# Performance work log

Hardware: AMD Instinct MI355X
Metric: run time of the kernel (lower is better)

The kernel has to match this reference:

```python
import jax, jax.numpy as jnp
import numpy as np
import math

NZ, NX, NY = 4, 2048, 2048
DX = DY = 4000.0


def dstI1D(x):
    # type-I discrete sine transform along last axis (ortho norm) via irfft
    n = x.shape[-1]
    pad = [(0, 0)] * (x.ndim - 1) + [(1, 1)]
    return jnp.fft.irfft(-1j * jnp.pad(x, pad), axis=-1, norm='ortho')[..., 1:n + 1]


def dstI2D(x):
    # DST-I over the last two axes
    x = dstI1D(x)
    x = jnp.swapaxes(dstI1D(jnp.swapaxes(x, -1, -2)), -1, -2)
    return x


def inverse_elliptic_dstI(f, helmholtz_dst):
    # DST-I is its own inverse with ortho norm: solve in spectral space
    return dstI2D(dstI2D(f) / helmholtz_dst)


def center_avg_2D(x):
    return 0.25 * (x[..., 1:, 1:] + x[..., 1:, :-1] + x[..., :-1, 1:] + x[..., :-1, :-1])


def _build_solver_constants(beta):
    # create_helmholtz_dst
    x, y = jnp.meshgrid(jnp.arange(1, NY), jnp.arange(1, NX), indexing='ij')
    L_mat = (2 * (jnp.cos(math.pi / NX * x) - 1) / DX ** 2
             + 2 * (jnp.cos(math.pi / NY * y) - 1) / DY ** 2)
    H_mat = (L_mat[None] - beta[:, None, None]).astype(jnp.float32)  # [Nz, Nx-1, Ny-1]
    # compute_homogeneous_solution
    ones_int = jnp.ones((NZ, NX - 1, NY - 1), jnp.float32)
    sol = inverse_elliptic_dstI(ones_int, H_mat)
    sol = jnp.pad(sol, ((0, 0), (1, 1), (1, 1)))  # [Nz, Nx+1, Ny+1]
    homsol = jnp.ones((NZ, NX + 1, NY + 1), jnp.float32) + sol * beta[:, None, None]
    homsol_mean = jnp.mean(center_avg_2D(homsol), axis=(-2, -1))  # mask = all ones
    return H_mat, homsol.astype(jnp.float32), homsol_mean.astype(jnp.float32)


def setup_inputs() -> dict:
    key = jax.random.key(0)
    k1, k2 = jax.random.split(key)
    q = jax.random.normal(k1, (NZ, NX - 1, NY - 1), jnp.float32)
    # mode<->layer change of basis (Mode2LayerTransformer): Cm2l = inv(Cl2m)
    A = jax.random.normal(k2, (NZ, NZ), jnp.float32) * 0.3 + jnp.eye(NZ, dtype=jnp.float32)
    Cl2m = A
    Cm2l = jnp.linalg.inv(A).astype(jnp.float32)
    # lambda_sq eigenvalues (1/deformation-radius^2), first barotropic mode ~ 0
    beta = jnp.array([0.0, 1.0e-9, 4.0e-9, 1.0e-8], jnp.float32)
    H_mat, homsol, homsol_mean = _build_solver_constants(beta)
    return {'q': q, 'Cl2m': Cl2m, 'Cm2l': Cm2l,
            'helmholtz_mat': H_mat, 'homsol': homsol, 'homsol_mean': homsol_mean}


def reference(q, Cl2m, Cm2l, helmholtz_mat, homsol, homsol_mean):
    # layer -> mode
    src_modes = jnp.einsum('ml,lxy->mxy', Cl2m, q)
    # spectral elliptic solve per mode (Nz batched over leading axis)
    psi_modes = inverse_elliptic_dstI(src_modes, helmholtz_mat)
    psi_modes = jnp.pad(psi_modes, ((0, 0), (1, 1), (1, 1)))  # [Nz, Nx+1, Ny+1]
    # homogeneous-solution correction to enforce zero mean
    psi_modes_mean = jnp.mean(center_avg_2D(psi_modes), axis=(-2, -1))
    alpha = -psi_modes_mean / homsol_mean
    psi_modes = psi_modes + alpha[:, None, None] * homsol
    # mode -> layer
    psi = jnp.einsum('lm,mxy->lxy', Cm2l, psi_modes)
    return psi
```

## Files before the change

kernel.cpp:

```cpp
#include <hip/hip_runtime.h>


typedef __attribute__((ext_vector_type(8))) short bf16x8;
typedef __attribute__((ext_vector_type(4))) float f32x4;
typedef __attribute__((ext_vector_type(8))) unsigned short ushort8;

#define LDS_SPACE __attribute__((address_space(3)))
#define GLB_SPACE __attribute__((address_space(1)))

__device__ __forceinline__ void gld_lds16(const unsigned short* g, unsigned short* l) {
  __builtin_amdgcn_global_load_lds((const GLB_SPACE void*)g, (LDS_SPACE void*)l, 16, 0, 0);
}

__device__ __forceinline__ bf16x8 ds_read128(const void* p) {
  bf16x8 r;
  const LDS_SPACE char* lp = (const LDS_SPACE char*)p;
  asm volatile("ds_read_b128 %0, %1" : "=v"(r) : "v"(lp));
  return r;
}

__device__ __forceinline__ float sinrev(float rev) {
  float r;
  asm("v_sin_f32 %0, %1" : "=v"(r) : "v"(rev));
  return r;
}

__device__ __forceinline__ unsigned short f2b(float f) {
  union { float f; unsigned u; } v; v.f = f;
  unsigned r = (v.u + 0x7fffu + ((v.u >> 16) & 1u)) >> 16;
  return (unsigned short)r;
}
__device__ __forceinline__ float b2f(unsigned short u) {
  union { unsigned u; float f; } v; v.u = ((unsigned)u) << 16;
  return v.f;
}

#define LGKM(N) asm volatile("s_waitcnt lgkmcnt(" #N ")" ::: "memory")
#define VMC(N)  asm volatile("s_waitcnt vmcnt(" #N ")" ::: "memory")
#define BAR()   __builtin_amdgcn_s_barrier()
#define SB0()   __builtin_amdgcn_sched_barrier(0)
#define PRIO1() __builtin_amdgcn_s_setprio(1)
#define PRIO0() __builtin_amdgcn_s_setprio(0)

__global__ __launch_bounds__(256)
void tables_kernel(unsigned short* __restrict__ T) {
  const int idx = blockIdx.x * 256 + threadIdx.x;
  const int tbl = idx >> 20, n = (idx >> 10) & 1023, k = idx & 1023;
  int a;
  if (tbl < 2) a = k;
  else a = (k < 512) ? 2 * k : (k < 1023 ? 2 * (k - 512) + 1 : 1023);
  const int cp1 = (tbl & 1) ? 2 * n + 2 : 2 * n + 1;
  const int ph = ((a + 1) * cp1) & 4095;
  const float v = 0.03125f * sinf(3.14159265358979323846f * (float)ph * (1.0f / 2048.0f));
  T[idx] = f2b(v);
}

__global__ __launch_bounds__(256)
void mix_fold(const float* __restrict__ q, const float* __restrict__ Cl2m,
              unsigned short* __restrict__ AE, unsigned short* __restrict__ AO) {
  const int idx = blockIdx.x * 256 + threadIdx.x;
  const int x = idx >> 10, u = idx & 1023;
  float c[16];
#pragma unroll
  for (int i = 0; i < 16; ++i) c[i] = Cl2m[i];
  float fe[4] = {0.f, 0.f, 0.f, 0.f}, fo[4] = {0.f, 0.f, 0.f, 0.f};
  if (x < 2047) {
#pragma unroll
    for (int l = 0; l < 4; ++l) {
      const size_t base = ((size_t)l * 2047 + x) * 2047;
      const float qa = q[base + u];
      const float qb = (u < 1023) ? q[base + 2046 - u] : 0.f;
      const float E = (u == 1023) ? qa : qa + qb;
      const float O = (u == 1023) ? 0.f : qa - qb;
#pragma unroll
      for (int m = 0; m < 4; ++m) { fe[m] += c[m * 4 + l] * E; fo[m] += c[m * 4 + l] * O; }
    }
  }
#pragma unroll
  for (int m = 0; m < 4; ++m) {
    AE[((size_t)m * 2048 + x) * 1024 + u] = f2b(fe[m]);
    AO[((size_t)m * 2048 + x) * 1024 + u] = f2b(fo[m]);
  }
}

template <int MAP>
__global__ __launch_bounds__(256)
void tfold(const unsigned short* __restrict__ in, unsigned short* __restrict__ outE,
           unsigned short* __restrict__ outO) {
  __shared__ unsigned short t1[64][72];
  __shared__ unsigned short t2[64][72];
  const size_t ib = (size_t)blockIdx.z * (2048u * 2048u);
  const size_t ob = (size_t)blockIdx.z * (2048u * 1024u);
  const int c0 = blockIdx.x * 64, u0 = blockIdx.y * 64;
  const int t = threadIdx.x;
  const int rr = t >> 3, cc = (t & 7) * 8;
#pragma unroll
  for (int ch = 0; ch < 2; ++ch) {
    const int r = ch * 32 + rr, u = u0 + r;
    const int r1 = (MAP == 0) ? u : (u < 512 ? u : 1024 + (u - 512));
    const int r2 = (MAP == 0) ? 2046 - u : (u < 512 ? 1023 - u : 2046 - (u - 512));
    ushort8 v1 = *(const ushort8*)&in[ib + (size_t)r1 * 2048 + c0 + cc];
    ushort8 v2 = *(const ushort8*)&in[ib + (size_t)r2 * 2048 + c0 + cc];
#pragma unroll
    for (int j = 0; j < 8; ++j) { t1[r][cc + j] = v1[j]; t2[r][cc + j] = v2[j]; }
  }
  __syncthreads();
#pragma unroll
  for (int ch = 0; ch < 2; ++ch) {
    const int r = ch * 32 + rr;
    ushort8 vE, vO;
#pragma unroll
    for (int j = 0; j < 8; ++j) {
      const int uu = u0 + cc + j;
      const float a = b2f(t1[cc + j][r]);
      const float b = b2f(t2[cc + j][r]);
      vE[j] = f2b((uu == 1023) ? a : a + b);
      vO[j] = f2b((uu == 1023) ? 0.f : a - b);
    }
    const size_t o = ob + (size_t)(c0 + r) * 1024 + u0 + cc;
    *(ushort8*)&outE[o] = vE;
    *(ushort8*)&outO[o] = vO;
  }
}

__global__ __launch_bounds__(256)
void fold_cols(const unsigned short* __restrict__ R, unsigned short* __restrict__ AE,
               unsigned short* __restrict__ AO) {
  const int idx = blockIdx.x * 256 + threadIdx.x;
  const int row = idx >> 10, u = idx & 1023;
  const int c1 = (u < 512) ? u : (u < 1023 ? 512 + u : 1535);
  const int c2 = (u < 512) ? 1023 - u : (u < 1023 ? 2558 - u : 1535);
  const float a = b2f(R[(size_t)row * 2048 + c1]);
  const float b = b2f(R[(size_t)row * 2048 + c2]);
  AE[(size_t)row * 1024 + u] = f2b((u == 1023) ? a : a + b);
  AO[(size_t)row * 1024 + u] = f2b((u == 1023) ? 0.f : a - b);
}

#define MFMA_BF16 __builtin_amdgcn_mfma_f32_16x16x32_bf16

template <int EPI>
__global__ __launch_bounds__(512, 2)
void gemm_eo(const unsigned short* __restrict__ A, const unsigned short* __restrict__ T,
             unsigned short* __restrict__ Cb, const float* __restrict__ H,
             float* __restrict__ sums) {
  __shared__ __align__(16) char lds[131072];
  const int bid = blockIdx.x;
  const int swz = (bid & 7) * 32 + (bid >> 3);
  const int h = swz & 1;
  const int bn = (swz >> 1) & 3, bm = swz >> 3;
  const int tid = threadIdx.x;
  const int lane = tid & 63, wave = tid >> 6;
  const int wr = wave >> 2, wc = wave & 3;
  const int lr = lane & 15, kg = lane >> 4;
  const int x7 = lr & 7;

  const unsigned short* gA = A + (size_t)h * 8388608u + (size_t)bm * 256 * 1024;
  const unsigned short* gB = T + (size_t)h * 1048576u + (size_t)bn * 256 * 1024;

  const int row0 = tid >> 3;
  const int slot = (tid & 7) ^ (row0 & 7);

  auto stage = [&](int kt, int c) {
    char* lc = lds + c * 65536;
    const size_t ko = (size_t)kt * 64 + slot * 8;
#pragma unroll
    for (int i = 0; i < 4; ++i)
      gld_lds16(gA + (size_t)(row0 + i * 64) * 1024 + ko,
                (unsigned short*)(lc + (tid + i * 512) * 16));
#pragma unroll
    for (int i = 0; i < 4; ++i)
      gld_lds16(gB + (size_t)(row0 + i * 64) * 1024 + ko,
                (unsigned short*)(lc + 32768 + (tid + i * 512) * 16));
  };

  f32x4 acc[8][4];
#pragma unroll
  for (int m = 0; m < 8; ++m)
#pragma unroll
    for (int n = 0; n < 4; ++n) acc[m][n] = (f32x4){0.f, 0.f, 0.f, 0.f};

  stage(0, 0);
  stage(1, 1);

  const int arow = wr * 128 + lr;
  const int brow = wc * 64 + lr;

  for (int t = 0; t < 16; ++t) {
    const char* la = lds + (t & 1) * 65536;
    const char* lb = la + 32768;
    if (t < 15) { VMC(8); } else { VMC(0); }
    BAR();

    bf16x8 al[4][2], ah[4][2], bl[2][2], bh[2][2];

#pragma unroll
    for (int m = 0; m < 4; ++m)
#pragma unroll
      for (int ks = 0; ks < 2; ++ks)
        al[m][ks] = ds_read128(la + (arow + m * 16) * 128 + (((ks * 4 + kg) ^ x7) << 4));
#pragma unroll
    for (int n = 0; n < 2; ++n)
#pragma unroll
      for (int ks = 0; ks < 2; ++ks)
        bl[n][ks] = ds_read128(lb + (brow + n * 16) * 128 + (((ks * 4 + kg) ^ x7) << 4));
    BAR();
    LGKM(0); SB0();
    PRIO1();
#pragma unroll
    for (int ks = 0; ks < 2; ++ks)
#pragma unroll
      for (int m = 0; m < 4; ++m)
#pragma unroll
        for (int n = 0; n < 2; ++n)
          acc[m][n] = MFMA_BF16(al[m][ks], bl[n][ks], acc[m][n], 0, 0, 0);
    PRIO0();

#pragma unroll
    for (int n = 0; n < 2; ++n)
#pragma unroll
      for (int ks = 0; ks < 2; ++ks)
        bh[n][ks] = ds_read128(lb + (brow + (n + 2) * 16) * 128 + (((ks * 4 + kg) ^ x7) << 4));
#pragma unroll
    for (int m = 0; m < 4; ++m)
#pragma unroll
      for (int ks = 0; ks < 2; ++ks)
        ah[m][ks] = ds_read128(la + (arow + (m + 4) * 16) * 128 + (((ks * 4 + kg) ^ x7) << 4));
    BAR();
    LGKM(8); SB0();
    PRIO1();
#pragma unroll
    for (int ks = 0; ks < 2; ++ks)
#pragma unroll
      for (int m = 0; m < 4; ++m)
#pragma unroll
        for (int n = 0; n < 2; ++n)
          acc[m][n + 2] = MFMA_BF16(al[m][ks], bh[n][ks], acc[m][n + 2], 0, 0, 0);
    PRIO0();

    BAR();
    LGKM(0); SB0();
    PRIO1();
#pragma unroll
    for (int ks = 0; ks < 2; ++ks)
#pragma unroll
      for (int m = 0; m < 4; ++m)
#pragma unroll
        for (int n = 0; n < 2; ++n)
          acc[m + 4][n + 2] = MFMA_BF16(ah[m][ks], bh[n][ks], acc[m + 4][n + 2], 0, 0, 0);
#pragma unroll
    for (int ks = 0; ks < 2; ++ks)
#pragma unroll
      for (int m = 0; m < 4; ++m)
#pragma unroll
        for (int n = 0; n < 2; ++n)
          acc[m + 4][n] = MFMA_BF16(ah[m][ks], bl[n][ks], acc[m + 4][n], 0, 0, 0);
    PRIO0();

    if (t < 14) stage(t + 2, t & 1);
  }

  LGKM(0); VMC(0);
  __syncthreads();

  float beta = 0.f, tA[4];
  bool iok[4] = {true, true, true, true};
  if (EPI == 1) {
    const float s1 = sinrev(1.0f / 8192.0f);
    beta = -5.0e-7f * s1 * s1 - H[(size_t)(bm >> 3) * 4190209u];
#pragma unroll
    for (int n = 0; n < 4; ++n) {
      const int ia = 2 * (bn * 256 + wc * 64 + n * 16 + lr) + h;
      iok[n] = ia < 2047;
      const float s = sinrev((float)(ia + 1) * (1.0f / 8192.0f));
      tA[n] = -2.5e-7f * s * s;
    }
  }

  float ssum = 0.f;
#pragma unroll
  for (int m = 0; m < 8; ++m) {
#pragma unroll
    for (int j = 0; j < 4; ++j) {
      const int row_l = wr * 128 + m * 16 + kg * 4 + j;
      float tB = 0.f;
      bool jok = true;
      if (EPI == 1) {
        const int jint = (bm * 256 + row_l) & 2047;
        const int j_true = 2 * (jint & 1023) + (jint >> 10);
        jok = j_true < 2047;
        const float s = sinrev((float)(j_true + 1) * (1.0f / 8192.0f));
        tB = -2.5e-7f * s * s;
      }
#pragma unroll
      for (int n = 0; n < 4; ++n) {
        const int col_l = wc * 64 + n * 16 + lr;
        float v = acc[m][n][j];
        if (EPI == 1) {
          const float Hv = tA[n] + tB - beta;
          float r = __builtin_amdgcn_rcpf(Hv);
          r = r * (2.0f - Hv * r);
          v = (iok[n] && jok) ? v * r : 0.f;
        }
        if (EPI == 2) ssum += v;
        const int byte = row_l * 512 + ((((col_l >> 3) ^ (row_l & 7)) << 4)) + (col_l & 7) * 2;
        *(unsigned short*)&lds[byte] = f2b(v);
      }
    }
  }
  __syncthreads();

  unsigned short* gC = Cb + (size_t)(bm * 256) * 2048 + h * 1024 + bn * 256;
#pragma unroll
  for (int p = 0; p < 16; ++p) {
    const int c = p * 512 + tid;
    const int r = c >> 5, c16 = c & 31;
    const bf16x8 vv = *(const bf16x8*)&lds[r * 512 + ((c16 ^ (r & 7)) << 4)];
    *(bf16x8*)&gC[(size_t)r * 2048 + c16 * 8] = vv;
  }

  if (EPI == 2) {
#pragma unroll
    for (int off = 32; off > 0; off >>= 1) ssum += __shfl_xor(ssum, off);
    if (lane == 0) atomicAdd(&sums[bm >> 3], ssum);
  }
}

__global__ __launch_bounds__(256)
void final_kernel(const unsigned short* __restrict__ V, const float* __restrict__ homsol,
                  const float* __restrict__ hm, const float* __restrict__ Cm2l,
                  const float* __restrict__ sums, float* __restrict__ out) {
  const int p = blockIdx.x * 256 + threadIdx.x;
  if (p >= 2049 * 2049) return;
  const int x = p / 2049, y = p - x * 2049;
  const bool interior = (x >= 1) && (x <= 2047) && (y >= 1) && (y <= 2047);
  int row = 0, col = 0;
  if (interior) {
    const int xt = x - 1, yt = y - 1;
    row = (xt & 1) ? 1024 + (xt >> 1) : (xt >> 1);
    col = (yt & 1) ? 1024 + (yt >> 1) : (yt >> 1);
  }
  float pm[4];
#pragma unroll
  for (int m = 0; m < 4; ++m) {
    float inner = 0.f;
    if (interior) inner = b2f(V[((size_t)m * 2048 + row) * 2048 + col]);
    const float alpha = -(sums[m] * (1.0f / 4194304.0f)) / hm[m];
    pm[m] = inner + alpha * homsol[(size_t)m * 4198401u + p];
  }
#pragma unroll
  for (int l = 0; l < 4; ++l) {
    out[(size_t)l * 4198401u + p] =
        Cm2l[l * 4 + 0] * pm[0] + Cm2l[l * 4 + 1] * pm[1] +
        Cm2l[l * 4 + 2] * pm[2] + Cm2l[l * 4 + 3] * pm[3];
  }
}

extern "C" void kernel_launch(void* const* d_in, const int* in_sizes, int n_in,
                              void* d_out, int out_size, void* d_ws, size_t ws_size,
                              hipStream_t stream) {
  const float* q     = (const float*)d_in[0];
  const float* Cl2m  = (const float*)d_in[1];
  const float* Cm2l  = (const float*)d_in[2];
  const float* H     = (const float*)d_in[3];
  const float* hom   = (const float*)d_in[4];
  const float* hmean = (const float*)d_in[5];
  float* out = (float*)d_out;

  char* ws = (char*)d_ws;
  unsigned short* Tb = (unsigned short*)ws;
  unsigned short* Aslot = (unsigned short*)(ws + 8388608u);
  unsigned short* Bslot = (unsigned short*)(ws + 41943040u);
  float* sums        = (float*)(ws + 75497472u);
  unsigned short* AO = Aslot + 8388608u;

  tables_kernel<<<16384, 256, 0, stream>>>(Tb);
  mix_fold<<<8192, 256, 0, stream>>>(q, Cl2m, Aslot, AO);
  hipMemsetAsync(sums, 0, 16, stream);

  const dim3 tg(32, 16, 4);
  gemm_eo<0><<<256, 512, 0, stream>>>(Aslot, Tb, Bslot, nullptr, nullptr);
  tfold<0><<<tg, 256, 0, stream>>>(Bslot, Aslot, AO);
  gemm_eo<1><<<256, 512, 0, stream>>>(Aslot, Tb, Bslot, H, nullptr);
  fold_cols<<<32768, 256, 0, stream>>>(Bslot, Aslot, AO);
  gemm_eo<0><<<256, 512, 0, stream>>>(Aslot, Tb + 2097152u, Bslot, nullptr, nullptr);
  tfold<1><<<tg, 256, 0, stream>>>(Bslot, Aslot, AO);
  gemm_eo<2><<<256, 512, 0, stream>>>(Aslot, Tb + 2097152u, Bslot, nullptr, sums);

  final_kernel<<<16401, 256, 0, stream>>>(Bslot, hom, hmean, Cm2l, sums, out);
}
```

Before: 278.7 us.

## Interleave half-tile global-to-LDS loads with MFMA quadrants in GEMM main loop

Restructures the gemm_eo main loop into an 8-iteration, two-buffer ping-pong. Global-to-LDS staging is split into half-tile chunks per matrix, and each chunk is issued between the four MFMA quadrant phases. Loads stay spread across the compute, rather than issued as one burst after all MFMAs, so memory traffic overlaps better with math. The cost is more barriers per iteration and a fragile ordering of buffer reuse: a buffer's halves are refilled while other waves may still be reading it. Near the end of the loop the clamped tile indices also cause redundant reloads of tile 15.

```diff
diff --git a/kernel.cpp b/kernel.cpp
--- a/kernel.cpp
+++ b/kernel.cpp
@@ -137,6 +137,36 @@
 }
 
 #define MFMA_BF16 __builtin_amdgcn_mfma_f32_16x16x32_bf16
+
+#define QUAD(AF, BF, MB, NB)                                            \
+  _Pragma("unroll")                                                     \
+  for (int ks = 0; ks < 2; ++ks)                                        \
+    _Pragma("unroll")                                                   \
+    for (int m = 0; m < 4; ++m)                                         \
+      _Pragma("unroll")                                                 \
+      for (int n = 0; n < 2; ++n)                                       \
+        acc[MB + m][NB + n] = MFMA_BF16(AF[m][ks], BF[n][ks], acc[MB + m][NB + n], 0, 0, 0);
+
+#define RD_A(DST, LA)                                                   \
+  _Pragma("unroll")                                                     \
+  for (int m = 0; m < 4; ++m)                                           \
+    _Pragma("unroll")                                                   \
+    for (int ks = 0; ks < 2; ++ks)                                      \
+      DST[m][ks] = ds_read128((LA) + (arow + m * 16) * 128 + (((ks * 4 + kg) ^ x7) << 4));
+
+#define RD_AH(DST, LA)                                                  \
+  _Pragma("unroll")                                                     \
+  for (int m = 0; m < 4; ++m)                                           \
+    _Pragma("unroll")                                                   \
+    for (int ks = 0; ks < 2; ++ks)                                      \
+      DST[m][ks] = ds_read128((LA) + (arow + (m + 4) * 16) * 128 + (((ks * 4 + kg) ^ x7) << 4));
+
+#define RD_B(DST, LB, NOFF)                                             \
+  _Pragma("unroll")                                                     \
+  for (int n = 0; n < 2; ++n)                                           \
+    _Pragma("unroll")                                                   \
+    for (int ks = 0; ks < 2; ++ks)                                      \
+      DST[n][ks] = ds_read128((LB) + (brow + (n + NOFF) * 16) * 128 + (((ks * 4 + kg) ^ x7) << 4));
 
 template <int EPI>
 __global__ __launch_bounds__(512, 2)
@@ -160,17 +190,15 @@
   const int row0 = tid >> 3;
   const int slot = (tid & 7) ^ (row0 & 7);
 
-  auto stage = [&](int kt, int c) {
-    char* lc = lds + c * 65536;
-    const size_t ko = (size_t)kt * 64 + slot * 8;
-#pragma unroll
-    for (int i = 0; i < 4; ++i)
-      gld_lds16(gA + (size_t)(row0 + i * 64) * 1024 + ko,
-                (unsigned short*)(lc + (tid + i * 512) * 16));
-#pragma unroll
-    for (int i = 0; i < 4; ++i)
-      gld_lds16(gB + (size_t)(row0 + i * 64) * 1024 + ko,
-                (unsigned short*)(lc + 32768 + (tid + i * 512) * 16));
+  auto stageHalf = [&](int kt, int buf, int mat, int hh) {
+    const unsigned short* g = mat ? gB : gA;
+    char* base = lds + buf * 65536 + mat * 32768;
+#pragma unroll
+    for (int c = 0; c < 2; ++c) {
+      const int row = hh * 128 + c * 64 + row0;
+      gld_lds16(g + (size_t)row * 1024 + (size_t)kt * 64 + slot * 8,
+                (unsigned short*)(base + row * 128 + (tid & 7) * 16));
+    }
   };
 
   f32x4 acc[8][4];
@@ -178,85 +206,66 @@
   for (int m = 0; m < 8; ++m)
 #pragma unroll
     for (int n = 0; n < 4; ++n) acc[m][n] = (f32x4){0.f, 0.f, 0.f, 0.f};
-
-  stage(0, 0);
-  stage(1, 1);
 
   const int arow = wr * 128 + lr;
   const int brow = wc * 64 + lr;
-
-  for (int t = 0; t < 16; ++t) {
-    const char* la = lds + (t & 1) * 65536;
-    const char* lb = la + 32768;
-    if (t < 15) { VMC(8); } else { VMC(0); }
-    BAR();
-
-    bf16x8 al[4][2], ah[4][2], bl[2][2], bh[2][2];
-
-#pragma unroll
-    for (int m = 0; m < 4; ++m)
-#pragma unroll
-      for (int ks = 0; ks < 2; ++ks)
-        al[m][ks] = ds_read128(la + (arow + m * 16) * 128 + (((ks * 4 + kg) ^ x7) << 4));
-#pragma unroll
-    for (int n = 0; n < 2; ++n)
-#pragma unroll
-      for (int ks = 0; ks < 2; ++ks)
-        bl[n][ks] = ds_read128(lb + (brow + n * 16) * 128 + (((ks * 4 + kg) ^ x7) << 4));
-    BAR();
-    LGKM(0); SB0();
-    PRIO1();
-#pragma unroll
-    for (int ks = 0; ks < 2; ++ks)
-#pragma unroll
-      for (int m = 0; m < 4; ++m)
-#pragma unroll
-        for (int n = 0; n < 2; ++n)
-          acc[m][n] = MFMA_BF16(al[m][ks], bl[n][ks], acc[m][n], 0, 0, 0);
-    PRIO0();
-
-#pragma unroll
-    for (int n = 0; n < 2; ++n)
-#pragma unroll
-      for (int ks = 0; ks < 2; ++ks)
-        bh[n][ks] = ds_read128(lb + (brow + (n + 2) * 16) * 128 + (((ks * 4 + kg) ^ x7) << 4));
-#pragma unroll
-    for (int m = 0; m < 4; ++m)
-#pragma unroll
-      for (int ks = 0; ks < 2; ++ks)
-        ah[m][ks] = ds_read128(la + (arow + (m + 4) * 16) * 128 + (((ks * 4 + kg) ^ x7) << 4));
-    BAR();
-    LGKM(8); SB0();
-    PRIO1();
-#pragma unroll
-    for (int ks = 0; ks < 2; ++ks)
-#pragma unroll
-      for (int m = 0; m < 4; ++m)
-#pragma unroll
-        for (int n = 0; n < 2; ++n)
-          acc[m][n + 2] = MFMA_BF16(al[m][ks], bh[n][ks], acc[m][n + 2], 0, 0, 0);
-    PRIO0();
-
-    BAR();
-    LGKM(0); SB0();
-    PRIO1();
-#pragma unroll
-    for (int ks = 0; ks < 2; ++ks)
-#pragma unroll
-      for (int m = 0; m < 4; ++m)
-#pragma unroll
-        for (int n = 0; n < 2; ++n)
-          acc[m + 4][n + 2] = MFMA_BF16(ah[m][ks], bh[n][ks], acc[m + 4][n + 2], 0, 0, 0);
-#pragma unroll
-    for (int ks = 0; ks < 2; ++ks)
-#pragma unroll
-      for (int m = 0; m < 4; ++m)
-#pragma unroll
-        for (int n = 0; n < 2; ++n)
-          acc[m + 4][n] = MFMA_BF16(ah[m][ks], bl[n][ks], acc[m + 4][n], 0, 0, 0);
-    PRIO0();
-
-    if (t < 14) stage(t + 2, t & 1);
+  const char* la0 = lds;            const char* lb0 = lds + 32768;
+  const char* la1 = lds + 65536;    const char* lb1 = lds + 98304;
+
+  bf16x8 al[4][2], ah[4][2], bl[2][2], bh[2][2];
+
+  stageHalf(0, 0, 0, 0); stageHalf(0, 0, 0, 1);
+  stageHalf(0, 0, 1, 0); stageHalf(0, 0, 1, 1);
+  stageHalf(1, 1, 1, 0); stageHalf(1, 1, 1, 1);
+  VMC(4);
+  BAR();
+
+  for (int i = 0; i < 8; ++i) {
+    const int v  = 2 * i + 1;
+    const int u2 = (2 * i + 2 < 16) ? 2 * i + 2 : 15;
+    const int v2 = (2 * i + 3 < 16) ? 2 * i + 3 : 15;
+
+    RD_A(al, la0); RD_B(bl, lb0, 0);
+    stageHalf(v, 1, 0, 0);
+    LGKM(8);
+    BAR(); LGKM(0); SB0();
+    PRIO1(); QUAD(al, bl, 0, 0); PRIO0(); BAR();
+
+    RD_B(bh, lb0, 2);
+    stageHalf(v, 1, 0, 1);
+    BAR(); LGKM(0); SB0();
+    PRIO1(); QUAD(al, bh, 0, 2); PRIO0(); BAR();
+
+    RD_AH(ah, la0);
+    stageHalf(u2, 0, 1, 0);
+    BAR(); LGKM(0); SB0();
+    PRIO1(); QUAD(ah, bh, 4, 2); PRIO0(); BAR();
+
+    stageHalf(u2, 0, 1, 1);
+    VMC(4);
+    BAR(); SB0();
+    PRIO1(); QUAD(ah, bl, 4, 0); PRIO0(); BAR();
+
+    RD_A(al, la1); RD_B(bl, lb1, 0);
+    stageHalf(u2, 0, 0, 0);
+    LGKM(8);
+    BAR(); LGKM(0); SB0();
+    PRIO1(); QUAD(al, bl, 0, 0); PRIO0(); BAR();
+
+    RD_B(bh, lb1, 2);
+    stageHalf(u2, 0, 0, 1);
+    BAR(); LGKM(0); SB0();
+    PRIO1(); QUAD(al, bh, 0, 2); PRIO0(); BAR();
+
+    RD_AH(ah, la1);
+    stageHalf(v2, 1, 1, 0);
+    BAR(); LGKM(0); SB0();
+    PRIO1(); QUAD(ah, bh, 4, 2); PRIO0(); BAR();
+
+    stageHalf(v2, 1, 1, 1);
+    VMC(4);
+    BAR(); SB0();
+    PRIO1(); QUAD(ah, bl, 4, 0); PRIO0(); BAR();
   }
 
   LGKM(0); VMC(0);
```

Result: slower. 315.4 us (+13.2%).

## Shrink GEMM tiles to 128x128 with 256 threads and K-step of 32

Applied to the files above, without the earlier changes.

Rewrites the even/odd DST GEMM kernel from 256x256 tiles with 512 threads and a 64-wide K step to 128x128 tiles with 256 threads and a 32-wide K step. The grid goes from 256 to 1024 blocks, with a new LDS swizzle and less LDS per block to allow more resident blocks. This aims to fill all compute units better than 256 blocks can. In exchange each block reuses less data, so global and LDS traffic per flop rises, and there are more barriers per unit of work.

```diff
diff --git a/kernel.cpp b/kernel.cpp
--- a/kernel.cpp
+++ b/kernel.cpp
@@ -139,124 +139,84 @@
 #define MFMA_BF16 __builtin_amdgcn_mfma_f32_16x16x32_bf16
 
 template <int EPI>
-__global__ __launch_bounds__(512, 2)
+__global__ __launch_bounds__(256, 3)
 void gemm_eo(const unsigned short* __restrict__ A, const unsigned short* __restrict__ T,
              unsigned short* __restrict__ Cb, const float* __restrict__ H,
              float* __restrict__ sums) {
-  __shared__ __align__(16) char lds[131072];
+  __shared__ __align__(16) char lds[32768];
   const int bid = blockIdx.x;
-  const int swz = (bid & 7) * 32 + (bid >> 3);
+  const int swz = (bid & 7) * 128 + (bid >> 3);
   const int h = swz & 1;
-  const int bn = (swz >> 1) & 3, bm = swz >> 3;
+  const int bn = (swz >> 1) & 7, bm = swz >> 4;
   const int tid = threadIdx.x;
   const int lane = tid & 63, wave = tid >> 6;
-  const int wr = wave >> 2, wc = wave & 3;
+  const int wr = wave >> 1, wc = wave & 1;
   const int lr = lane & 15, kg = lane >> 4;
-  const int x7 = lr & 7;
-
-  const unsigned short* gA = A + (size_t)h * 8388608u + (size_t)bm * 256 * 1024;
-  const unsigned short* gB = T + (size_t)h * 1048576u + (size_t)bn * 256 * 1024;
-
-  const int row0 = tid >> 3;
-  const int slot = (tid & 7) ^ (row0 & 7);
+  const int x2 = (lr ^ (lr >> 2)) & 3;
+
+  const unsigned short* gA = A + (size_t)h * 8388608u + (size_t)bm * 128 * 1024;
+  const unsigned short* gB = T + (size_t)h * 1048576u + (size_t)bn * 128 * 1024;
 
   auto stage = [&](int kt, int c) {
-    char* lc = lds + c * 65536;
-    const size_t ko = (size_t)kt * 64 + slot * 8;
-#pragma unroll
-    for (int i = 0; i < 4; ++i)
-      gld_lds16(gA + (size_t)(row0 + i * 64) * 1024 + ko,
-                (unsigned short*)(lc + (tid + i * 512) * 16));
-#pragma unroll
-    for (int i = 0; i < 4; ++i)
-      gld_lds16(gB + (size_t)(row0 + i * 64) * 1024 + ko,
-                (unsigned short*)(lc + 32768 + (tid + i * 512) * 16));
+    char* lcA = lds + c * 8192;
+    char* lcB = lds + 16384 + c * 8192;
+    const int ko = kt * 32;
+#pragma unroll
+    for (int i = 0; i < 2; ++i) {
+      const int ps = tid + i * 256;
+      const int row = ps >> 2;
+      const int k16 = (ps & 3) ^ ((row ^ (row >> 2)) & 3);
+      gld_lds16(gA + (size_t)row * 1024 + ko + k16 * 8,
+                (unsigned short*)(lcA + ps * 16));
+    }
+#pragma unroll
+    for (int i = 0; i < 2; ++i) {
+      const int ps = tid + i * 256;
+      const int row = ps >> 2;
+      const int k16 = (ps & 3) ^ ((row ^ (row >> 2)) & 3);
+      gld_lds16(gB + (size_t)row * 1024 + ko + k16 * 8,
+                (unsigned short*)(lcB + ps * 16));
+    }
   };
 
-  f32x4 acc[8][4];
-#pragma unroll
-  for (int m = 0; m < 8; ++m)
+  f32x4 acc[4][4];
+#pragma unroll
+  for (int m = 0; m < 4; ++m)
 #pragma unroll
     for (int n = 0; n < 4; ++n) acc[m][n] = (f32x4){0.f, 0.f, 0.f, 0.f};
 
   stage(0, 0);
   stage(1, 1);
 
-  const int arow = wr * 128 + lr;
+  const int arow = wr * 64 + lr;
   const int brow = wc * 64 + lr;
-
-  for (int t = 0; t < 16; ++t) {
-    const char* la = lds + (t & 1) * 65536;
-    const char* lb = la + 32768;
-    if (t < 15) { VMC(8); } else { VMC(0); }
+  const int rdoff = ((kg ^ x2) << 4);
+
+  for (int t = 0; t < 32; ++t) {
+    const char* la = lds + (t & 1) * 8192;
+    const char* lb = lds + 16384 + (t & 1) * 8192;
+    if (t < 31) { VMC(4); } else { VMC(0); }
     BAR();
 
-    bf16x8 al[4][2], ah[4][2], bl[2][2], bh[2][2];
-
-#pragma unroll
-    for (int m = 0; m < 4; ++m)
-#pragma unroll
-      for (int ks = 0; ks < 2; ++ks)
-        al[m][ks] = ds_read128(la + (arow + m * 16) * 128 + (((ks * 4 + kg) ^ x7) << 4));
-#pragma unroll
-    for (int n = 0; n < 2; ++n)
-#pragma unroll
-      for (int ks = 0; ks < 2; ++ks)
-        bl[n][ks] = ds_read128(lb + (brow + n * 16) * 128 + (((ks * 4 + kg) ^ x7) << 4));
+    bf16x8 av[4], bv[4];
+#pragma unroll
+    for (int i = 0; i < 4; ++i)
+      av[i] = ds_read128(la + (arow + i * 16) * 64 + rdoff);
+#pragma unroll
+    for (int j = 0; j < 4; ++j)
+      bv[j] = ds_read128(lb + (brow + j * 16) * 64 + rdoff);
+    LGKM(0); SB0();
     BAR();
-    LGKM(0); SB0();
+
+    if (t < 30) stage(t + 2, t & 1);
+
     PRIO1();
 #pragma unroll
-    for (int ks = 0; ks < 2; ++ks)
-#pragma unroll
-      for (int m = 0; m < 4; ++m)
-#pragma unroll
-        for (int n = 0; n < 2; ++n)
-          acc[m][n] = MFMA_BF16(al[m][ks], bl[n][ks], acc[m][n], 0, 0, 0);
+    for (int mi = 0; mi < 4; ++mi)
+#pragma unroll
+      for (int ni = 0; ni < 4; ++ni)
+        acc[mi][ni] = MFMA_BF16(av[mi], bv[ni], acc[mi][ni], 0, 0, 0);
     PRIO0();
-
-#pragma unroll
-    for (int n = 0; n < 2; ++n)
-#pragma unroll
-      for (int ks = 0; ks < 2; ++ks)
-        bh[n][ks] = ds_read128(lb + (brow + (n + 2) * 16) * 128 + (((ks * 4 + kg) ^ x7) << 4));
-#pragma unroll
-    for (int m = 0; m < 4; ++m)
-#pragma unroll
-      for (int ks = 0; ks < 2; ++ks)
-        ah[m][ks] = ds_read128(la + (arow + (m + 4) * 16) * 128 + (((ks * 4 + kg) ^ x7) << 4));
-    BAR();
-    LGKM(8); SB0();
-    PRIO1();
-#pragma unroll
-    for (int ks = 0; ks < 2; ++ks)
-#pragma unroll
-      for (int m = 0; m < 4; ++m)
-#pragma unroll
-        for (int n = 0; n < 2; ++n)
-          acc[m][n + 2] = MFMA_BF16(al[m][ks], bh[n][ks], acc[m][n + 2], 0, 0, 0);
-    PRIO0();
-
-    BAR();
-    LGKM(0); SB0();
-    PRIO1();
-#pragma unroll
-    for (int ks = 0; ks < 2; ++ks)
-#pragma unroll
-      for (int m = 0; m < 4; ++m)
-#pragma unroll
-        for (int n = 0; n < 2; ++n)
-          acc[m + 4][n + 2] = MFMA_BF16(ah[m][ks], bh[n][ks], acc[m + 4][n + 2], 0, 0, 0);
-#pragma unroll
-    for (int ks = 0; ks < 2; ++ks)
-#pragma unroll
-      for (int m = 0; m < 4; ++m)
-#pragma unroll
-        for (int n = 0; n < 2; ++n)
-          acc[m + 4][n] = MFMA_BF16(ah[m][ks], bl[n][ks], acc[m + 4][n], 0, 0, 0);
-    PRIO0();
-
-    if (t < 14) stage(t + 2, t & 1);
   }
 
   LGKM(0); VMC(0);
@@ -266,10 +226,10 @@
   bool iok[4] = {true, true, true, true};
   if (EPI == 1) {
     const float s1 = sinrev(1.0f / 8192.0f);
-    beta = -5.0e-7f * s1 * s1 - H[(size_t)(bm >> 3) * 4190209u];
+    beta = -5.0e-7f * s1 * s1 - H[(size_t)(bm >> 4) * 4190209u];
 #pragma unroll
     for (int n = 0; n < 4; ++n) {
-      const int ia = 2 * (bn * 256 + wc * 64 + n * 16 + lr) + h;
+      const int ia = 2 * (bn * 128 + wc * 64 + n * 16 + lr) + h;
       iok[n] = ia < 2047;
       const float s = sinrev((float)(ia + 1) * (1.0f / 8192.0f));
       tA[n] = -2.5e-7f * s * s;
@@ -278,14 +238,14 @@
 
   float ssum = 0.f;
 #pragma unroll
-  for (int m = 0; m < 8; ++m) {
+  for (int m = 0; m < 4; ++m) {
 #pragma unroll
     for (int j = 0; j < 4; ++j) {
-      const int row_l = wr * 128 + m * 16 + kg * 4 + j;
+      const int row_l = wr * 64 + m * 16 + kg * 4 + j;
       float tB = 0.f;
       bool jok = true;
       if (EPI == 1) {
-        const int jint = (bm * 256 + row_l) & 2047;
+        const int jint = (bm * 128 + row_l) & 2047;
         const int j_true = 2 * (jint & 1023) + (jint >> 10);
         jok = j_true < 2047;
         const float s = sinrev((float)(j_true + 1) * (1.0f / 8192.0f));
@@ -302,26 +262,26 @@
           v = (iok[n] && jok) ? v * r : 0.f;
         }
         if (EPI == 2) ssum += v;
-        const int byte = row_l * 512 + ((((col_l >> 3) ^ (row_l & 7)) << 4)) + (col_l & 7) * 2;
+        const int byte = row_l * 256 + ((((col_l >> 3) ^ (row_l & 7)) << 4)) + (col_l & 7) * 2;
         *(unsigned short*)&lds[byte] = f2b(v);
       }
     }
   }
   __syncthreads();
 
-  unsigned short* gC = Cb + (size_t)(bm * 256) * 2048 + h * 1024 + bn * 256;
-#pragma unroll
-  for (int p = 0; p < 16; ++p) {
-    const int c = p * 512 + tid;
-    const int r = c >> 5, c16 = c & 31;
-    const bf16x8 vv = *(const bf16x8*)&lds[r * 512 + ((c16 ^ (r & 7)) << 4)];
+  unsigned short* gC = Cb + (size_t)(bm * 128) * 2048 + h * 1024 + bn * 128;
+#pragma unroll
+  for (int p = 0; p < 8; ++p) {
+    const int c = p * 256 + tid;
+    const int r = c >> 4, c16 = c & 15;
+    const bf16x8 vv = *(const bf16x8*)&lds[r * 256 + ((c16 ^ (r & 7)) << 4)];
     *(bf16x8*)&gC[(size_t)r * 2048 + c16 * 8] = vv;
   }
 
   if (EPI == 2) {
 #pragma unroll
     for (int off = 32; off > 0; off >>= 1) ssum += __shfl_xor(ssum, off);
-    if (lane == 0) atomicAdd(&sums[bm >> 3], ssum);
+    if (lane == 0) atomicAdd(&sums[bm >> 4], ssum);
   }
 }
 
@@ -378,13 +338,13 @@
   hipMemsetAsync(sums, 0, 16, stream);
 
   const dim3 tg(32, 16, 4);
-  gemm_eo<0><<<256, 512, 0, stream>>>(Aslot, Tb, Bslot, nullptr, nullptr);
+  gemm_eo<0><<<1024, 256, 0, stream>>>(Aslot, Tb, Bslot, nullptr, nullptr);
   tfold<0><<<tg, 256, 0, stream>>>(Bslot, Aslot, AO);
-  gemm_eo<1><<<256, 512, 0, stream>>>(Aslot, Tb, Bslot, H, nullptr);
+  gemm_eo<1><<<1024, 256, 0, stream>>>(Aslot, Tb, Bslot, H, nullptr);
   fold_cols<<<32768, 256, 0, stream>>>(Bslot, Aslot, AO);
-  gemm_eo<0><<<256, 512, 0, stream>>>(Aslot, Tb + 2097152u, Bslot, nullptr, nullptr);
+  gemm_eo<0><<<1024, 256, 0, stream>>>(Aslot, Tb + 2097152u, Bslot, nullptr, nullptr);
   tfold<1><<<tg, 256, 0, stream>>>(Bslot, Aslot, AO);
-  gemm_eo<2><<<256, 512, 0, stream>>>(Aslot, Tb + 2097152u, Bslot, nullptr, sums);
+  gemm_eo<2><<<1024, 256, 0, stream>>>(Aslot, Tb + 2097152u, Bslot, nullptr, sums);
 
   final_kernel<<<16401, 256, 0, stream>>>(Bslot, hom, hmean, Cm2l, sums, out);
 }
```

After: 316.8 us. 13.7% more time.
